# Kernel optimization log

Measured on AMD Instinct MI355X. Metric: run time of the kernel, lower is better.

The kernel has to match this reference:

```python
import jax, jax.numpy as jnp
import numpy as np

B, S, C = 4, 2048, 1024
N_HEAD = 16
HEAD_DIM = C // N_HEAD


def setup_inputs() -> dict:
    key = jax.random.key(0)
    k1, k2, k3, k4, k5 = jax.random.split(key, 5)
    scale = 1.0 / np.sqrt(C)
    x = jax.random.normal(k1, (B, S, C), dtype=jnp.float32)
    W_attn = jax.random.normal(k2, (C, 3 * C), dtype=jnp.float32) * scale
    b_attn = jax.random.normal(k3, (3 * C,), dtype=jnp.float32) * 0.02
    W_proj = jax.random.normal(k4, (C, C), dtype=jnp.float32) * scale
    b_proj = jax.random.normal(k5, (C,), dtype=jnp.float32) * 0.02
    return {"x": x, "W_attn": W_attn, "b_attn": b_attn, "W_proj": W_proj, "b_proj": b_proj}


def reference(x, W_attn, b_attn, W_proj, b_proj):
    Bx, Sx, Cx = x.shape
    qkv = x @ W_attn + b_attn                      # [B,S,3C]
    q, k, v = jnp.split(qkv, 3, axis=-1)
    # [B,S,C] -> [B,H,S,D]
    def heads(t):
        return t.reshape(Bx, Sx, N_HEAD, HEAD_DIM).transpose(0, 2, 1, 3)
    q, k, v = heads(q), heads(k), heads(v)
    scores = jnp.einsum('bhqd,bhkd->bhqk', q, k) / np.sqrt(HEAD_DIM)
    causal = jnp.tril(jnp.ones((Sx, Sx), dtype=bool))
    scores = jnp.where(causal[None, None], scores, -jnp.inf)
    attn = jax.nn.softmax(scores, axis=-1)
    out = jnp.einsum('bhqk,bhkd->bhqd', attn, v)   # [B,H,S,D]
    out = out.transpose(0, 2, 1, 3).reshape(Bx, Sx, Cx)
    return out @ W_proj + b_proj
```

## Files before the change

### kernel.cpp

```cpp
#include <hip/hip_runtime.h>
#include <hip/hip_bf16.h>

typedef __hip_bfloat16 bf16;
#define NEG_BIG (-3.0e38f)

typedef __bf16 bf16x8 __attribute__((ext_vector_type(8)));
typedef float  f32x4  __attribute__((ext_vector_type(4)));

__device__ inline void load8_f32(const float* p, float* o) {
  float4 a = *reinterpret_cast<const float4*>(p);
  float4 b = *reinterpret_cast<const float4*>(p + 4);
  o[0]=a.x; o[1]=a.y; o[2]=a.z; o[3]=a.w;
  o[4]=b.x; o[5]=b.y; o[6]=b.z; o[7]=b.w;
}

__device__ inline int swz8(int row, int kg) { return ((kg ^ ((row >> 3) & 3)) << 3); }

__global__ __launch_bounds__(1024)
void qkv_f(const float* __restrict__ X, const float* __restrict__ W,
           const float* __restrict__ bias,
           bf16* __restrict__ q, bf16* __restrict__ k, bf16* __restrict__ v)
{
  __shared__ __align__(16) unsigned char smem[67584];
  bf16 (*As)[40] = reinterpret_cast<bf16 (*)[40]>(smem);
  bf16 (*Bs)[48] = reinterpret_cast<bf16 (*)[48]>(smem + 40960);

  const int t   = threadIdx.x;
  const int f   = blockIdx.x;
  const int xcd = f & 7, j = f >> 3;
  const int bm  = xcd * 4 + (j & 3);
  const int bn  = j >> 2;
  const int gm0 = bm * 256, gn0 = bn * 128;
  const int w    = t >> 6, lane = t & 63;
  const int g    = lane >> 4, l15 = lane & 15;
  const int wr   = w >> 2, wc = w & 3;

  const int am  = t >> 2, akg = t & 3;
  const int bnr = t & 127, kg4 = t >> 7;

  f32x4 acc[4][2];
#pragma unroll
  for (int i = 0; i < 4; i++)
#pragma unroll
    for (int jj = 0; jj < 2; jj++) acc[i][jj] = {0.f, 0.f, 0.f, 0.f};

  const float* aptr = X + (size_t)(gm0 + am) * 1024 + akg * 8;
  const float* wptr = W + (size_t)(kg4 * 4) * 3072 + gn0 + bnr;

  float a32_0[8], a32_1[8], wb_0[4], wb_1[4];
  load8_f32(aptr, a32_0);
#pragma unroll
  for (int kk = 0; kk < 4; kk++) wb_0[kk] = wptr[kk * 3072];
  aptr += 32; wptr += 32 * 3072;
  load8_f32(aptr, a32_1);
#pragma unroll
  for (int kk = 0; kk < 4; kk++) wb_1[kk] = wptr[kk * 3072];

  for (int kt = 0; kt < 1024; kt += 64) {
    {
      __align__(16) bf16 ab[8];
      __align__(8)  bf16 bb[4];
#pragma unroll
      for (int i = 0; i < 8; i++) ab[i] = __float2bfloat16(a32_0[i]);
#pragma unroll
      for (int i = 0; i < 4; i++) bb[i] = __float2bfloat16(wb_0[i]);
      *reinterpret_cast<uint4*>(&As[am][swz8(am, akg)]) = *reinterpret_cast<const uint4*>(ab);
      *reinterpret_cast<uint2*>(&Bs[bnr][swz8(bnr, kg4 >> 1) + (kg4 & 1) * 4]) =
          *reinterpret_cast<const uint2*>(bb);
      if (kt + 64 < 1024) {
        aptr += 32; wptr += 32 * 3072;
        load8_f32(aptr, a32_0);
#pragma unroll
        for (int kk = 0; kk < 4; kk++) wb_0[kk] = wptr[kk * 3072];
      }
      __syncthreads();
      bf16x8 af[4], bfr[2];
#pragma unroll
      for (int mt = 0; mt < 4; mt++) {
        const int r_ = wr * 64 + mt * 16 + l15;
        af[mt] = *reinterpret_cast<const bf16x8*>(&As[r_][swz8(r_, g)]);
      }
#pragma unroll
      for (int nt = 0; nt < 2; nt++) {
        const int r_ = wc * 32 + nt * 16 + l15;
        bfr[nt] = *reinterpret_cast<const bf16x8*>(&Bs[r_][swz8(r_, g)]);
      }
      __builtin_amdgcn_s_setprio(1);
#pragma unroll
      for (int mt = 0; mt < 4; mt++)
#pragma unroll
        for (int nt = 0; nt < 2; nt++)
          acc[mt][nt] = __builtin_amdgcn_mfma_f32_16x16x32_bf16(af[mt], bfr[nt], acc[mt][nt], 0, 0, 0);
      __builtin_amdgcn_s_setprio(0);
    }
    {
      __align__(16) bf16 ab[8];
      __align__(8)  bf16 bb[4];
#pragma unroll
      for (int i = 0; i < 8; i++) ab[i] = __float2bfloat16(a32_1[i]);
#pragma unroll
      for (int i = 0; i < 4; i++) bb[i] = __float2bfloat16(wb_1[i]);
      *reinterpret_cast<uint4*>(&As[256 + am][swz8(am, akg)]) = *reinterpret_cast<const uint4*>(ab);
      *reinterpret_cast<uint2*>(&Bs[128 + bnr][swz8(bnr, kg4 >> 1) + (kg4 & 1) * 4]) =
          *reinterpret_cast<const uint2*>(bb);
      if (kt + 96 < 1024) {
        aptr += 32; wptr += 32 * 3072;
        load8_f32(aptr, a32_1);
#pragma unroll
        for (int kk = 0; kk < 4; kk++) wb_1[kk] = wptr[kk * 3072];
      }
      __syncthreads();
      bf16x8 af[4], bfr[2];
#pragma unroll
      for (int mt = 0; mt < 4; mt++) {
        const int r_ = wr * 64 + mt * 16 + l15;
        af[mt] = *reinterpret_cast<const bf16x8*>(&As[256 + r_][swz8(r_, g)]);
      }
#pragma unroll
      for (int nt = 0; nt < 2; nt++) {
        const int r_ = wc * 32 + nt * 16 + l15;
        bfr[nt] = *reinterpret_cast<const bf16x8*>(&Bs[128 + r_][swz8(r_, g)]);
      }
      __builtin_amdgcn_s_setprio(1);
#pragma unroll
      for (int mt = 0; mt < 4; mt++)
#pragma unroll
        for (int nt = 0; nt < 2; nt++)
          acc[mt][nt] = __builtin_amdgcn_mfma_f32_16x16x32_bf16(af[mt], bfr[nt], acc[mt][nt], 0, 0, 0);
      __builtin_amdgcn_s_setprio(0);
    }
  }

  const int which = gn0 >> 10;
  if (which == 2) {
    bf16 (*Vep)[264] = reinterpret_cast<bf16 (*)[264]>(smem);
    __syncthreads();
#pragma unroll
    for (int nt = 0; nt < 2; nt++) {
      const int c = wc * 32 + nt * 16 + l15;
      const float bvs = bias[gn0 + c];
#pragma unroll
      for (int mt = 0; mt < 4; mt++)
#pragma unroll
        for (int r = 0; r < 4; r++) {
          const int s = wr * 64 + mt * 16 + g * 4 + r;
          Vep[c][s] = __float2bfloat16(acc[mt][nt][r] + bvs);
        }
    }
    __syncthreads();
    const int c   = t >> 3, tl = t & 7;
    const int bb2 = gm0 >> 11, sl0 = gm0 & 2047;
    const int hh  = ((gn0 - 2048) >> 6) + (c >> 6), d = c & 63;
    bf16* vrow = v + ((size_t)(bb2 * 16 + hh) * 64 + d) * 2048 + sl0;
#pragma unroll
    for (int it = 0; it < 4; it++) {
      const int s_off = tl * 8 + it * 64;
      *reinterpret_cast<uint4*>(vrow + s_off) =
          *reinterpret_cast<const uint4*>(&Vep[c][s_off]);
    }
  } else {
    bf16* dst = (which == 0) ? q : k;
#pragma unroll
    for (int nt = 0; nt < 2; nt++) {
      const int gc  = gn0 + wc * 32 + nt * 16 + l15;
      const float bvs = bias[gc];
      const int cc = gc & 1023;
      const int hh = cc >> 6, d = cc & 63;
#pragma unroll
      for (int mt = 0; mt < 4; mt++)
#pragma unroll
        for (int r = 0; r < 4; r++) {
          const int gr = gm0 + wr * 64 + mt * 16 + g * 4 + r;
          const int bb2 = gr >> 11, s = gr & 2047;
          float val = acc[mt][nt][r] + bvs;
          if (which == 0) val *= 0.125f;
          dst[((size_t)(bb2 * 16 + hh) * 2048 + s) * 64 + d] = __float2bfloat16(val);
        }
    }
  }
}

__global__ __launch_bounds__(256)
void attn_f(bf16* __restrict__ qo, const bf16* __restrict__ k, const bf16* __restrict__ v)
{
  __shared__ __align__(16) bf16 Ks[64][72];
  __shared__ __align__(16) bf16 Vt[64][72];
  __shared__ __align__(16) bf16 Ps[4][16][72];

  const int t    = threadIdx.x;
  const int f    = blockIdx.x;
  const int xcd  = f & 7;
  const int j    = f >> 3;
  const int hb   = xcd + 8 * (j >> 4);
  const int qt0  = j & 15;
  const int b    = hb >> 4, h = hb & 15;
  const size_t basebh = (size_t)(b * 16 + h) * 2048 * 64;

  const int w    = t >> 6;
  const int lane = t & 63;
  const int g    = lane >> 4;
  const int l15  = lane & 15;

  const int sr = t >> 3;
  const int sc = (t & 7) * 8;
  const bf16* kbase = k + basebh;
  const bf16* vbase = v + basebh;

#pragma unroll 1
  for (int pass = 0; pass < 2; ++pass) {
    const int qt = pass ? qt0 : (31 - qt0);
    const int qb = qt * 64 + w * 16;

    const bf16* qrow = qo + basebh + (size_t)(qb + l15) * 64;
    bf16x8 qf0 = *reinterpret_cast<const bf16x8*>(qrow + g * 8);
    bf16x8 qf1 = *reinterpret_cast<const bf16x8*>(qrow + 32 + g * 8);

    f32x4 acc[4] = {{0,0,0,0},{0,0,0,0},{0,0,0,0},{0,0,0,0}};
    float m_run = NEG_BIG, l_run = 0.f;

    uint4 kreg0, kreg1, vreg0, vreg1;
    {
      kreg0 = *reinterpret_cast<const uint4*>(kbase + (size_t)(sr) * 64 + sc);
      kreg1 = *reinterpret_cast<const uint4*>(kbase + (size_t)(32 + sr) * 64 + sc);
      vreg0 = *reinterpret_cast<const uint4*>(vbase + (size_t)sr * 2048 + sc);
      vreg1 = *reinterpret_cast<const uint4*>(vbase + (size_t)(32 + sr) * 2048 + sc);
    }

    for (int ct = 0; ct <= qt; ++ct) {
      const int kv0 = ct * 64;
      __syncthreads();
      *reinterpret_cast<uint4*>(&Ks[sr][sc])      = kreg0;
      *reinterpret_cast<uint4*>(&Ks[32 + sr][sc]) = kreg1;
      *reinterpret_cast<uint4*>(&Vt[sr][sc])      = vreg0;
      *reinterpret_cast<uint4*>(&Vt[32 + sr][sc]) = vreg1;
      if (ct < qt) {
        const int nv0 = kv0 + 64;
        kreg0 = *reinterpret_cast<const uint4*>(kbase + (size_t)(nv0 + sr) * 64 + sc);
        kreg1 = *reinterpret_cast<const uint4*>(kbase + (size_t)(nv0 + 32 + sr) * 64 + sc);
        vreg0 = *reinterpret_cast<const uint4*>(vbase + (size_t)sr * 2048 + nv0 + sc);
        vreg1 = *reinterpret_cast<const uint4*>(vbase + (size_t)(32 + sr) * 2048 + nv0 + sc);
      }
      __syncthreads();

      f32x4 st[4];
#pragma unroll
      for (int kt = 0; kt < 4; ++kt) {
        const int kr = kt * 16 + l15;
        bf16x8 kf0 = *reinterpret_cast<const bf16x8*>(&Ks[kr][g * 8]);
        bf16x8 kf1 = *reinterpret_cast<const bf16x8*>(&Ks[kr][32 + g * 8]);
        f32x4 c4 = {0,0,0,0};
        c4 = __builtin_amdgcn_mfma_f32_16x16x32_bf16(kf0, qf0, c4, 0, 0, 0);
        c4 = __builtin_amdgcn_mfma_f32_16x16x32_bf16(kf1, qf1, c4, 0, 0, 0);
        st[kt] = c4;
      }
      if (ct == qt) {
        const int qg = qb + l15;
#pragma unroll
        for (int kt = 0; kt < 4; ++kt)
#pragma unroll
          for (int r = 0; r < 4; ++r)
            if (kv0 + kt * 16 + g * 4 + r > qg) st[kt][r] = NEG_BIG;
      }

      float mc = NEG_BIG;
#pragma unroll
      for (int kt = 0; kt < 4; ++kt)
#pragma unroll
        for (int r = 0; r < 4; ++r) mc = fmaxf(mc, st[kt][r]);
      mc = fmaxf(mc, __shfl_xor(mc, 16));
      mc = fmaxf(mc, __shfl_xor(mc, 32));
      if (!__all(mc - m_run <= 8.0f)) {
        const float mn = fmaxf(m_run, mc);
        const float alpha = __expf(m_run - mn);
        m_run = mn;
        l_run *= alpha;
#pragma unroll
        for (int r = 0; r < 4; ++r) {
          const float ar = __shfl(alpha, g * 4 + r, 64);
#pragma unroll
          for (int dt = 0; dt < 4; ++dt) acc[dt][r] *= ar;
        }
      }
      float ps = 0.f;
#pragma unroll
      for (int kt = 0; kt < 4; ++kt)
#pragma unroll
        for (int r = 0; r < 4; ++r) {
          const float pv = __expf(st[kt][r] - m_run);
          st[kt][r] = pv;
          ps += pv;
        }
      ps += __shfl_xor(ps, 16);
      ps += __shfl_xor(ps, 32);
      l_run += ps;

#pragma unroll
      for (int kt = 0; kt < 4; ++kt) {
        union { bf16 hh[4]; uint2 u; } pk;
        pk.hh[0] = __float2bfloat16(st[kt][0]);
        pk.hh[1] = __float2bfloat16(st[kt][1]);
        pk.hh[2] = __float2bfloat16(st[kt][2]);
        pk.hh[3] = __float2bfloat16(st[kt][3]);
        *reinterpret_cast<uint2*>(&Ps[w][l15][kt * 16 + g * 4]) = pk.u;
      }
      __builtin_amdgcn_sched_barrier(0);

#pragma unroll
      for (int kc = 0; kc < 2; ++kc) {
        bf16x8 pf = *reinterpret_cast<const bf16x8*>(&Ps[w][l15][kc * 32 + g * 8]);
#pragma unroll
        for (int dt = 0; dt < 4; ++dt) {
          bf16x8 vf = *reinterpret_cast<const bf16x8*>(&Vt[dt * 16 + l15][kc * 32 + g * 8]);
          acc[dt] = __builtin_amdgcn_mfma_f32_16x16x32_bf16(pf, vf, acc[dt], 0, 0, 0);
        }
      }
    }

    const float linv = 1.f / l_run;
    float inv[4];
#pragma unroll
    for (int r = 0; r < 4; ++r) inv[r] = __shfl(linv, g * 4 + r, 64);
    bf16* op = qo + basebh;
#pragma unroll
    for (int dt = 0; dt < 4; ++dt)
#pragma unroll
      for (int r = 0; r < 4; ++r)
        op[(size_t)(qb + g * 4 + r) * 64 + dt * 16 + l15] =
            __float2bfloat16(acc[dt][r] * inv[r]);
  }
}

__global__ __launch_bounds__(1024)
void proj_f(const bf16* __restrict__ A, const float* __restrict__ W,
            const float* __restrict__ bias, float* __restrict__ out)
{
  __shared__ __align__(16) bf16 As[2][256][40];
  __shared__ __align__(16) bf16 Bs[2][128][48];
  const int t   = threadIdx.x;
  const int f   = blockIdx.x;
  const int xcd = f & 7, j = f >> 3;
  const int bm  = xcd * 4 + (j & 3);
  const int bn  = j >> 2;
  const int gm0 = bm * 256, gn0 = bn * 128;
  const int w    = t >> 6, lane = t & 63;
  const int g    = lane >> 4, l15 = lane & 15;
  const int wr   = w >> 2, wc = w & 3;

  const int am  = t >> 2, akg = t & 3;
  const int bnr = t & 127, kg4 = t >> 7;

  const int gr_l = gm0 + am;
  const int bb_l = gr_l >> 11, s_l = gr_l & 2047;
  const bf16* abase = A + (size_t)bb_l * 2097152 + (size_t)s_l * 64;

  f32x4 acc[4][2];
#pragma unroll
  for (int i = 0; i < 4; i++)
#pragma unroll
    for (int jj = 0; jj < 2; jj++) acc[i][jj] = {0.f, 0.f, 0.f, 0.f};

  const float* wptr = W + (size_t)(kg4 * 4) * 1024 + gn0 + bnr;

  uint4 a0_0, a0_1;
  float wb_0[4], wb_1[4];
  {
    const int c0 = akg * 8;
    a0_0 = *reinterpret_cast<const uint4*>(abase + (size_t)(c0 >> 6) * 131072 + (c0 & 63));
    const int c1 = 32 + akg * 8;
    a0_1 = *reinterpret_cast<const uint4*>(abase + (size_t)(c1 >> 6) * 131072 + (c1 & 63));
  }
#pragma unroll
  for (int kk = 0; kk < 4; kk++) wb_0[kk] = wptr[kk * 1024];
  wptr += 32 * 1024;
#pragma unroll
  for (int kk = 0; kk < 4; kk++) wb_1[kk] = wptr[kk * 1024];

  for (int kt = 0; kt < 1024; kt += 64) {
    {
      __align__(8) bf16 bb[4];
#pragma unroll
      for (int i = 0; i < 4; i++) bb[i] = __float2bfloat16(wb_0[i]);
      *reinterpret_cast<uint4*>(&As[0][am][swz8(am, akg)]) = a0_0;
      *reinterpret_cast<uint2*>(&Bs[0][bnr][swz8(bnr, kg4 >> 1) + (kg4 & 1) * 4]) =
          *reinterpret_cast<const uint2*>(bb);
      if (kt + 64 < 1024) {
        const int c0 = kt + 64 + akg * 8;
        a0_0 = *reinterpret_cast<const uint4*>(abase + (size_t)(c0 >> 6) * 131072 + (c0 & 63));
        wptr += 32 * 1024;
#pragma unroll
        for (int kk = 0; kk < 4; kk++) wb_0[kk] = wptr[kk * 1024];
      }
      __syncthreads();
      bf16x8 af[4], bfr[2];
#pragma unroll
      for (int mt = 0; mt < 4; mt++) {
        const int r_ = wr * 64 + mt * 16 + l15;
        af[mt] = *reinterpret_cast<const bf16x8*>(&As[0][r_][swz8(r_, g)]);
      }
#pragma unroll
      for (int nt = 0; nt < 2; nt++) {
        const int r_ = wc * 32 + nt * 16 + l15;
        bfr[nt] = *reinterpret_cast<const bf16x8*>(&Bs[0][r_][swz8(r_, g)]);
      }
      __builtin_amdgcn_s_setprio(1);
#pragma unroll
      for (int mt = 0; mt < 4; mt++)
#pragma unroll
        for (int nt = 0; nt < 2; nt++)
          acc[mt][nt] = __builtin_amdgcn_mfma_f32_16x16x32_bf16(af[mt], bfr[nt], acc[mt][nt], 0, 0, 0);
      __builtin_amdgcn_s_setprio(0);
    }
    {
      __align__(8) bf16 bb[4];
#pragma unroll
      for (int i = 0; i < 4; i++) bb[i] = __float2bfloat16(wb_1[i]);
      *reinterpret_cast<uint4*>(&As[1][am][swz8(am, akg)]) = a0_1;
      *reinterpret_cast<uint2*>(&Bs[1][bnr][swz8(bnr, kg4 >> 1) + (kg4 & 1) * 4]) =
          *reinterpret_cast<const uint2*>(bb);
      if (kt + 96 < 1024) {
        const int c1 = kt + 96 + akg * 8;
        a0_1 = *reinterpret_cast<const uint4*>(abase + (size_t)(c1 >> 6) * 131072 + (c1 & 63));
        wptr += 32 * 1024;
#pragma unroll
        for (int kk = 0; kk < 4; kk++) wb_1[kk] = wptr[kk * 1024];
      }
      __syncthreads();
      bf16x8 af[4], bfr[2];
#pragma unroll
      for (int mt = 0; mt < 4; mt++) {
        const int r_ = wr * 64 + mt * 16 + l15;
        af[mt] = *reinterpret_cast<const bf16x8*>(&As[1][r_][swz8(r_, g)]);
      }
#pragma unroll
      for (int nt = 0; nt < 2; nt++) {
        const int r_ = wc * 32 + nt * 16 + l15;
        bfr[nt] = *reinterpret_cast<const bf16x8*>(&Bs[1][r_][swz8(r_, g)]);
      }
      __builtin_amdgcn_s_setprio(1);
#pragma unroll
      for (int mt = 0; mt < 4; mt++)
#pragma unroll
        for (int nt = 0; nt < 2; nt++)
          acc[mt][nt] = __builtin_amdgcn_mfma_f32_16x16x32_bf16(af[mt], bfr[nt], acc[mt][nt], 0, 0, 0);
      __builtin_amdgcn_s_setprio(0);
    }
  }

#pragma unroll
  for (int nt = 0; nt < 2; nt++) {
    const int gc = gn0 + wc * 32 + nt * 16 + l15;
    const float bvs = bias[gc];
#pragma unroll
    for (int mt = 0; mt < 4; mt++)
#pragma unroll
      for (int r = 0; r < 4; r++) {
        const int gr = gm0 + wr * 64 + mt * 16 + g * 4 + r;
        out[(size_t)gr * 1024 + gc] = acc[mt][nt][r] + bvs;
      }
  }
}

extern "C" void kernel_launch(void* const* d_in, const int* in_sizes, int n_in,
                              void* d_out, int out_size, void* d_ws, size_t ws_size,
                              hipStream_t stream)
{
  const float *x = nullptr, *W_attn = nullptr, *b_attn = nullptr,
              *W_proj = nullptr, *b_proj = nullptr;
  for (int i = 0; i < n_in; i++) {
    switch (in_sizes[i]) {
      case 8388608: x      = (const float*)d_in[i]; break;
      case 3145728: W_attn = (const float*)d_in[i]; break;
      case 3072:    b_attn = (const float*)d_in[i]; break;
      case 1048576: W_proj = (const float*)d_in[i]; break;
      case 1024:    b_proj = (const float*)d_in[i]; break;
      default: break;
    }
  }
  if (!x || !W_attn || !b_attn || !W_proj || !b_proj) {
    x = (const float*)d_in[0]; W_attn = (const float*)d_in[1];
    b_attn = (const float*)d_in[2]; W_proj = (const float*)d_in[3];
    b_proj = (const float*)d_in[4];
  }
  float* out = (float*)d_out;

  const size_t NE = 8388608;
  bf16* qb = (bf16*)d_ws;
  bf16* kb = (bf16*)d_out;
  bf16* vb = kb + NE;

  qkv_f <<<dim3(768), 1024, 0, stream>>>(x, W_attn, b_attn, qb, kb, vb);
  attn_f<<<dim3(1024), 256, 0, stream>>>(qb, kb, vb);
  proj_f<<<dim3(256), 1024, 0, stream>>>(qb, W_proj, b_proj, out);
}
```

Baseline: 186.1 us.

## Load K and V MFMA fragments directly from global memory, drop LDS staging

The attention kernel no longer stages K and V tiles through shared memory with a register prefetch and two block barriers per tile. Each wave now loads its MFMA operand fragments straight from global memory (K row-major, V already transposed) into registers. This removes the LDS writes and reads and the block-wide syncs per KV tile. In exchange, all four waves separately load the same K/V data through the caches, and there is no longer any prefetch of the next tile to hide global-load latency.

New measurement: 341.2 us. 83.3% more time.

```diff
diff --git a/kernel.cpp b/kernel.cpp
--- a/kernel.cpp
+++ b/kernel.cpp
@@ -183,8 +183,6 @@
 __global__ __launch_bounds__(256)
 void attn_f(bf16* __restrict__ qo, const bf16* __restrict__ k, const bf16* __restrict__ v)
 {
-  __shared__ __align__(16) bf16 Ks[64][72];
-  __shared__ __align__(16) bf16 Vt[64][72];
   __shared__ __align__(16) bf16 Ps[4][16][72];
 
   const int t    = threadIdx.x;
@@ -201,8 +199,6 @@
   const int g    = lane >> 4;
   const int l15  = lane & 15;
 
-  const int sr = t >> 3;
-  const int sc = (t & 7) * 8;
   const bf16* kbase = k + basebh;
   const bf16* vbase = v + basebh;
 
@@ -218,41 +214,35 @@
     f32x4 acc[4] = {{0,0,0,0},{0,0,0,0},{0,0,0,0},{0,0,0,0}};
     float m_run = NEG_BIG, l_run = 0.f;
 
-    uint4 kreg0, kreg1, vreg0, vreg1;
-    {
-      kreg0 = *reinterpret_cast<const uint4*>(kbase + (size_t)(sr) * 64 + sc);
-      kreg1 = *reinterpret_cast<const uint4*>(kbase + (size_t)(32 + sr) * 64 + sc);
-      vreg0 = *reinterpret_cast<const uint4*>(vbase + (size_t)sr * 2048 + sc);
-      vreg1 = *reinterpret_cast<const uint4*>(vbase + (size_t)(32 + sr) * 2048 + sc);
-    }
-
+#pragma unroll 1
     for (int ct = 0; ct <= qt; ++ct) {
       const int kv0 = ct * 64;
-      __syncthreads();
-      *reinterpret_cast<uint4*>(&Ks[sr][sc])      = kreg0;
-      *reinterpret_cast<uint4*>(&Ks[32 + sr][sc]) = kreg1;
-      *reinterpret_cast<uint4*>(&Vt[sr][sc])      = vreg0;
-      *reinterpret_cast<uint4*>(&Vt[32 + sr][sc]) = vreg1;
-      if (ct < qt) {
-        const int nv0 = kv0 + 64;
-        kreg0 = *reinterpret_cast<const uint4*>(kbase + (size_t)(nv0 + sr) * 64 + sc);
-        kreg1 = *reinterpret_cast<const uint4*>(kbase + (size_t)(nv0 + 32 + sr) * 64 + sc);
-        vreg0 = *reinterpret_cast<const uint4*>(vbase + (size_t)sr * 2048 + nv0 + sc);
-        vreg1 = *reinterpret_cast<const uint4*>(vbase + (size_t)(32 + sr) * 2048 + nv0 + sc);
-      }
-      __syncthreads();
+
+      const bf16* krow = kbase + (size_t)(kv0 + l15) * 64 + g * 8;
+      bf16x8 kf0[4], kf1[4];
+#pragma unroll
+      for (int kt = 0; kt < 4; ++kt) {
+        kf0[kt] = *reinterpret_cast<const bf16x8*>(krow + kt * 16 * 64);
+        kf1[kt] = *reinterpret_cast<const bf16x8*>(krow + kt * 16 * 64 + 32);
+      }
 
       f32x4 st[4];
 #pragma unroll
       for (int kt = 0; kt < 4; ++kt) {
-        const int kr = kt * 16 + l15;
-        bf16x8 kf0 = *reinterpret_cast<const bf16x8*>(&Ks[kr][g * 8]);
-        bf16x8 kf1 = *reinterpret_cast<const bf16x8*>(&Ks[kr][32 + g * 8]);
         f32x4 c4 = {0,0,0,0};
-        c4 = __builtin_amdgcn_mfma_f32_16x16x32_bf16(kf0, qf0, c4, 0, 0, 0);
-        c4 = __builtin_amdgcn_mfma_f32_16x16x32_bf16(kf1, qf1, c4, 0, 0, 0);
+        c4 = __builtin_amdgcn_mfma_f32_16x16x32_bf16(kf0[kt], qf0, c4, 0, 0, 0);
+        c4 = __builtin_amdgcn_mfma_f32_16x16x32_bf16(kf1[kt], qf1, c4, 0, 0, 0);
         st[kt] = c4;
       }
+
+      const bf16* vrow = vbase + (size_t)l15 * 2048 + kv0 + g * 8;
+      bf16x8 vf0[4], vf1[4];
+#pragma unroll
+      for (int dt = 0; dt < 4; ++dt) {
+        vf0[dt] = *reinterpret_cast<const bf16x8*>(vrow + (size_t)dt * 16 * 2048);
+        vf1[dt] = *reinterpret_cast<const bf16x8*>(vrow + (size_t)dt * 16 * 2048 + 32);
+      }
+
       if (ct == qt) {
         const int qg = qb + l15;
 #pragma unroll
@@ -305,13 +295,13 @@
       }
       __builtin_amdgcn_sched_barrier(0);
 
-#pragma unroll
-      for (int kc = 0; kc < 2; ++kc) {
-        bf16x8 pf = *reinterpret_cast<const bf16x8*>(&Ps[w][l15][kc * 32 + g * 8]);
+      {
+        bf16x8 pf0 = *reinterpret_cast<const bf16x8*>(&Ps[w][l15][g * 8]);
+        bf16x8 pf1 = *reinterpret_cast<const bf16x8*>(&Ps[w][l15][32 + g * 8]);
 #pragma unroll
         for (int dt = 0; dt < 4; ++dt) {
-          bf16x8 vf = *reinterpret_cast<const bf16x8*>(&Vt[dt * 16 + l15][kc * 32 + g * 8]);
-          acc[dt] = __builtin_amdgcn_mfma_f32_16x16x32_bf16(pf, vf, acc[dt], 0, 0, 0);
+          acc[dt] = __builtin_amdgcn_mfma_f32_16x16x32_bf16(pf0, vf0[dt], acc[dt], 0, 0, 0);
+          acc[dt] = __builtin_amdgcn_mfma_f32_16x16x32_bf16(pf1, vf1[dt], acc[dt], 0, 0, 0);
         }
       }
     }
```
